# Kernel optimization log

Hardware: AMD Instinct MI355X
Metric: run time of the kernel (lower is better)

Reference implementation:

```python
import jax, jax.numpy as jnp
import numpy as np

D_MODEL = 1024
N_EXPERTS = 8
TOP_K = 2


def setup_inputs() -> dict:
    key = jax.random.key(0)
    ks = jax.random.split(key, 8)
    d, e = D_MODEL, N_EXPERTS
    s = 1.0 / np.sqrt(d)
    return {
        "x": jax.random.normal(ks[0], (4, 2048, d), dtype=jnp.float32),
        "W_gate": jax.random.uniform(ks[1], (d, e), jnp.float32, -s, s),
        "b_gate": jax.random.uniform(ks[2], (e,), jnp.float32, -s, s),
        "W1": jax.random.uniform(ks[3], (e, d, d), jnp.float32, -s, s),
        "b1": jax.random.uniform(ks[4], (e, d), jnp.float32, -s, s),
        "W2": jax.random.uniform(ks[5], (e, d, d), jnp.float32, -s, s),
        "b2": jax.random.uniform(ks[6], (e, d), jnp.float32, -s, s),
    }


def reference(x, W_gate, b_gate, W1, b1, W2, b2):
    B, T, d = x.shape
    xf = x.reshape(-1, d)  # [N, d], N = B*T
    # gating: raw linear scores, top-k selection; top-k raw scores are the
    # combine weights (original applies no softmax to gate scores)
    scores = xf @ W_gate + b_gate  # [N, E]
    topk_val, topk_idx = jax.lax.top_k(scores, TOP_K)  # [N, K]
    # scatter top-k weights into dense [N, E] combine matrix (indices distinct)
    onehot = jax.nn.one_hot(topk_idx, N_EXPERTS, dtype=xf.dtype)  # [N, K, E]
    w = jnp.einsum("nk,nke->ne", topk_val, onehot)  # [N, E]
    # run every expert MLP densely, then mask-combine (static shapes under jit)
    h = jax.nn.relu(jnp.einsum("nd,edh->neh", xf, W1) + b1)  # [N, E, d]
    y = jnp.einsum("neh,ehd->ned", h, W2) + b2  # [N, E, d]
    out = jnp.einsum("ned,ne->nd", y, w)  # weighted combine over experts
    return out.reshape(B, T, d)
```

## Files before the change

kernel.cpp:

```cpp
#include <hip/hip_runtime.h>
#include <hip/hip_bf16.h>


#define NTOK   8192
#define DM     1024
#define NE     8
#define BM     128
#define NSLOT  (NTOK * 2)
#define PADCAP (NSLOT + NE * BM)
#define MAXTILES (PADCAP / BM)

typedef __attribute__((ext_vector_type(8))) short  bf16x8;
typedef __attribute__((ext_vector_type(4))) float  f32x4;
typedef __attribute__((ext_vector_type(8))) unsigned short u16x8;

__device__ __forceinline__ unsigned short f2bf(float f) {
    union { float f; unsigned u; } v; v.f = f;
    unsigned r = v.u + 0x7fffu + ((v.u >> 16) & 1u);
    return (unsigned short)(r >> 16);
}

__device__ __forceinline__ void load_lds16(const ushort* g, ushort* l) {
    __builtin_amdgcn_global_load_lds(
        (const __attribute__((address_space(1))) unsigned int*)g,
        (__attribute__((address_space(3))) unsigned int*)l,
        16, 0, 0);
}

__global__ __launch_bounds__(256) void k_transpose2(const float* __restrict__ W1,
                                                    const float* __restrict__ W2,
                                                    ushort* __restrict__ w1t,
                                                    ushort* __restrict__ w2t,
                                                    int* __restrict__ counts) {
    int tid = threadIdx.x;
    if (blockIdx.x == 0 && blockIdx.y == 0 && blockIdx.z == 0 && tid < 16)
        counts[tid] = 0;
    int ez = blockIdx.z;
    const float* W = (ez < 8 ? W1 : W2) + (size_t)(ez & 7) * DM * DM;
    ushort* Wt = (ez < 8 ? w1t : w2t) + (size_t)(ez & 7) * DM * DM;
    __shared__ float t[64][65];
    int kt = blockIdx.y * 64, nt = blockIdx.x * 64;
    int r16 = tid >> 4, c4 = (tid & 15) * 4;
#pragma unroll
    for (int p = 0; p < 4; p++) {
        int k = p * 16 + r16;
        float4 v = *(const float4*)&W[(size_t)(kt + k) * DM + nt + c4];
        t[k][c4] = v.x; t[k][c4 + 1] = v.y; t[k][c4 + 2] = v.z; t[k][c4 + 3] = v.w;
    }
    __syncthreads();
    int n = tid >> 2, kb = (tid & 3) * 16;
#pragma unroll
    for (int h = 0; h < 2; h++) {
        int k0 = kb + h * 8;
        u16x8 o;
#pragma unroll
        for (int i = 0; i < 8; i++) o[i] = f2bf(t[k0 + i][n]);
        *(u16x8*)&Wt[(size_t)(nt + n) * DM + kt + k0] = o;
    }
}

__global__ __launch_bounds__(256) void k_gate(const float* __restrict__ x,
                                              const float* __restrict__ Wg,
                                              const float* __restrict__ bg,
                                              ushort* __restrict__ xb,
                                              int* __restrict__ tok_e,
                                              float* __restrict__ tok_w,
                                              int* __restrict__ counts,
                                              float* __restrict__ out,
                                              int* __restrict__ slot_token) {
    __shared__ float wgT[NE][DM];
    __shared__ int cnt[NE];
    int tid = threadIdx.x;
    if (tid < NE) cnt[tid] = 0;
    {
        float4 z4 = {0.f, 0.f, 0.f, 0.f};
        float4* orow = (float4*)(out + (size_t)blockIdx.x * 16 * DM);
#pragma unroll
        for (int i = 0; i < 16; i++) orow[i * 256 + tid] = z4;
        int s0 = blockIdx.x * (PADCAP / 512);
        for (int i = tid; i < PADCAP / 512; i += 256) slot_token[s0 + i] = -1;
    }
    for (int i = tid; i < DM * NE; i += 256) {
        int d = i >> 3, e = i & 7;
        wgT[e][d] = Wg[i];
    }
    __syncthreads();
    int wave = tid >> 6, lane = tid & 63;
    int n0 = (blockIdx.x * 4 + wave) * 4;
    const float4* xr[4];
#pragma unroll
    for (int t = 0; t < 4; t++) xr[t] = (const float4*)(x + (size_t)(n0 + t) * DM);

    float acc[4][NE];
#pragma unroll
    for (int t = 0; t < 4; t++)
#pragma unroll
        for (int e = 0; e < NE; e++) acc[t][e] = 0.f;

#pragma unroll
    for (int j = 0; j < 4; j++) {
        float4 xv[4];
#pragma unroll
        for (int t = 0; t < 4; t++) xv[t] = xr[t][j * 64 + lane];
#pragma unroll
        for (int t = 0; t < 4; t++) {
            ushort4 o;
            o.x = f2bf(xv[t].x); o.y = f2bf(xv[t].y);
            o.z = f2bf(xv[t].z); o.w = f2bf(xv[t].w);
            ((ushort4*)xb)[(size_t)(n0 + t) * (DM / 4) + j * 64 + lane] = o;
        }
#pragma unroll
        for (int e = 0; e < NE; e++) {
            float4 wv = ((const float4*)&wgT[e][0])[j * 64 + lane];
#pragma unroll
            for (int t = 0; t < 4; t++) {
                acc[t][e] += xv[t].x * wv.x + xv[t].y * wv.y
                           + xv[t].z * wv.z + xv[t].w * wv.w;
            }
        }
    }
#pragma unroll
    for (int t = 0; t < 4; t++)
#pragma unroll
        for (int e = 0; e < NE; e++) {
#pragma unroll
            for (int off = 32; off >= 1; off >>= 1)
                acc[t][e] += __shfl_xor(acc[t][e], off);
        }
    if (lane < 4) {
        int t = lane, n = n0 + t;
        float sc[NE];
#pragma unroll
        for (int e = 0; e < NE; e++) sc[e] = acc[t][e] + bg[e];
        int e0 = 0; float v0 = sc[0];
#pragma unroll
        for (int e = 1; e < NE; e++) if (sc[e] > v0) { v0 = sc[e]; e0 = e; }
        int e1 = -1; float v1 = -3.0e38f;
#pragma unroll
        for (int e = 0; e < NE; e++) if (e != e0 && sc[e] > v1) { v1 = sc[e]; e1 = e; }
        tok_e[2 * n] = e0;     tok_w[2 * n] = v0;
        tok_e[2 * n + 1] = e1; tok_w[2 * n + 1] = v1;
        atomicAdd(&cnt[e0], 1);
        atomicAdd(&cnt[e1], 1);
    }
    __syncthreads();
    if (tid < NE) atomicAdd(&counts[tid], cnt[tid]);
}

__global__ __launch_bounds__(256) void k_fillplan(const int* __restrict__ tok_e,
                                                  const float* __restrict__ tok_w,
                                                  const int* __restrict__ counts,
                                                  int* __restrict__ cursor,
                                                  int* __restrict__ slot_token,
                                                  float* __restrict__ slot_w,
                                                  int* __restrict__ tile_e,
                                                  int* __restrict__ tile_b,
                                                  int* __restrict__ ntiles) {
    __shared__ int lcnt[NE], lbase[NE];
    int tid = threadIdx.x;
    if (tid < NE) lcnt[tid] = 0;
    __syncthreads();
    int n = blockIdx.x * 256 + tid;
    int e0 = tok_e[2 * n],     e1 = tok_e[2 * n + 1];
    float w0 = tok_w[2 * n],   w1 = tok_w[2 * n + 1];
    int p0 = atomicAdd(&lcnt[e0], 1);
    int p1 = atomicAdd(&lcnt[e1], 1);
    __syncthreads();
    if (tid < NE) lbase[tid] = atomicAdd(&cursor[tid], lcnt[tid]);
    if (blockIdx.x == 0 && tid == 32) {
        int t = 0, o2 = 0;
        for (int e = 0; e < NE; e++) {
            int nt = (counts[e] + BM - 1) / BM;
            for (int i = 0; i < nt; i++) { tile_e[t] = e; tile_b[t] = o2 + i * BM; t++; }
            o2 += nt * BM;
        }
        *ntiles = t;
    }
    __syncthreads();
    int base[NE]; int off = 0;
#pragma unroll
    for (int e = 0; e < NE; e++) {
        base[e] = off;
        off += ((counts[e] + BM - 1) / BM) * BM;
    }
    int s0 = base[e0] + lbase[e0] + p0;
    slot_token[s0] = n; slot_w[s0] = w0;
    int s1 = base[e1] + lbase[e1] + p1;
    slot_token[s1] = n; slot_w[s1] = w1;
}

template <int PHASE>
__global__ __launch_bounds__(256) void k_gemm(const ushort* __restrict__ A,
                                              const ushort* __restrict__ Wt,
                                              const float* __restrict__ bias,
                                              const int* __restrict__ slot_token,
                                              const float* __restrict__ slot_w,
                                              const int* __restrict__ tile_e,
                                              const int* __restrict__ tile_b,
                                              const int* __restrict__ ntiles,
                                              ushort* __restrict__ Hout,
                                              float* __restrict__ out) {
    int flat = blockIdx.x;
    int wid = (flat & 7) * (MAXTILES * 2) + (flat >> 3);
    int t = wid >> 4;
    if (t >= *ntiles) return;
    int ncol0 = (wid & 15) << 6;
    int e = tile_e[t];
    int sbase = tile_b[t];

    __shared__ ushort As[2][4096];
    __shared__ ushort Bs[2][2048];

    int tid = threadIdx.x;
    int wave = tid >> 6, lane = tid & 63, quad = lane >> 4, lm = lane & 15;
    int wm = wave >> 1, wn = wave & 1;

    const ushort* Wte = Wt + (size_t)e * DM * DM;

    int sr = lane >> 2;
    int gseg = (lane & 3) ^ ((lane >> 4) & 3);
    const ushort* aptr[2];
    const ushort* bptr;
#pragma unroll
    for (int ci = 0; ci < 2; ci++) {
        int row = (wave * 2 + ci) * 16 + sr;
        int ar;
        if (PHASE == 1) {
            ar = slot_token[sbase + row];
            if (ar < 0) ar = 0;
        } else {
            ar = sbase + row;
        }
        aptr[ci] = A + (size_t)ar * DM + gseg * 8;
    }
    {
        int brow = wave * 16 + sr;
        bptr = Wte + (size_t)(ncol0 + brow) * DM + gseg * 8;
    }

    f32x4 acc[4][2];
#pragma unroll
    for (int i = 0; i < 4; i++)
#pragma unroll
        for (int j = 0; j < 2; j++) acc[i][j] = (f32x4){0.f, 0.f, 0.f, 0.f};

    int asel = ((quad ^ (lm >> 2)) & 3) * 8;
    int abase = (wm * 64 + lm) * 32 + asel;
    int bbase = (wn * 32 + lm) * 32 + asel;

#define ISSUE(buf, koff)                                              \
    do {                                                              \
        load_lds16(aptr[0] + (koff), &As[(buf)][(wave * 2 + 0) * 512]); \
        load_lds16(aptr[1] + (koff), &As[(buf)][(wave * 2 + 1) * 512]); \
        load_lds16(bptr + (koff), &Bs[(buf)][wave * 512]);            \
    } while (0)

#define COMPUTE(buf)                                                          \
    do {                                                                      \
        const ushort* Ab = As[(buf)];                                         \
        const ushort* Bb = Bs[(buf)];                                         \
        bf16x8 av[4], bv[2];                                                  \
        _Pragma("unroll")                                                     \
        for (int f = 0; f < 4; f++) av[f] = *(const bf16x8*)&Ab[abase + f * 512]; \
        _Pragma("unroll")                                                     \
        for (int f = 0; f < 2; f++) bv[f] = *(const bf16x8*)&Bb[bbase + f * 512]; \
        __builtin_amdgcn_s_setprio(1);                                        \
        _Pragma("unroll")                                                     \
        for (int fm = 0; fm < 4; fm++)                                        \
            _Pragma("unroll")                                                 \
            for (int fn = 0; fn < 2; fn++)                                    \
                acc[fm][fn] = __builtin_amdgcn_mfma_f32_16x16x32_bf16(        \
                    av[fm], bv[fn], acc[fm][fn], 0, 0, 0);                    \
        __builtin_amdgcn_s_setprio(0);                                        \
    } while (0)

    ISSUE(0, 0);
#pragma unroll 2
    for (int it = 0; it < 32; ++it) {
        if (it < 31) {
            ISSUE((it + 1) & 1, (it + 1) * 32);
            __builtin_amdgcn_s_waitcnt(0x0F73);
        } else {
            __builtin_amdgcn_s_waitcnt(0x0F70);
        }
        __builtin_amdgcn_s_barrier();
        __builtin_amdgcn_sched_barrier(0);
        COMPUTE(it & 1);
        __builtin_amdgcn_sched_barrier(0);
        __builtin_amdgcn_s_waitcnt(0xC07F);
        __builtin_amdgcn_s_barrier();
    }
#undef ISSUE
#undef COMPUTE

#pragma unroll
    for (int fm = 0; fm < 4; fm++) {
        int rowg = wm * 64 + fm * 16 + quad * 4;
        if (PHASE == 1) {
#pragma unroll
            for (int fn = 0; fn < 2; fn++) {
                int col = ncol0 + wn * 32 + fn * 16 + lm;
                float bv2 = bias[e * DM + col];
#pragma unroll
                for (int r = 0; r < 4; r++) {
                    float v = acc[fm][fn][r] + bv2;
                    v = fmaxf(v, 0.f);
                    Hout[(size_t)(sbase + rowg + r) * DM + col] = f2bf(v);
                }
            }
        } else {
            int tk[4]; float wv[4];
#pragma unroll
            for (int r = 0; r < 4; r++) {
                tk[r] = slot_token[sbase + rowg + r];
                wv[r] = slot_w[sbase + rowg + r];
            }
#pragma unroll
            for (int fn = 0; fn < 2; fn++) {
                int col = ncol0 + wn * 32 + fn * 16 + lm;
                float bv2 = bias[e * DM + col];
#pragma unroll
                for (int r = 0; r < 4; r++) {
                    if (tk[r] >= 0) {
                        float v = wv[r] * (acc[fm][fn][r] + bv2);
                        atomicAdd(&out[(size_t)tk[r] * DM + col], v);
                    }
                }
            }
        }
    }
}

extern "C" void kernel_launch(void* const* d_in, const int* in_sizes, int n_in,
                              void* d_out, int out_size, void* d_ws, size_t ws_size,
                              hipStream_t stream) {
    const float* x  = (const float*)d_in[0];
    const float* Wg = (const float*)d_in[1];
    const float* bg = (const float*)d_in[2];
    const float* W1 = (const float*)d_in[3];
    const float* b1 = (const float*)d_in[4];
    const float* W2 = (const float*)d_in[5];
    const float* b2 = (const float*)d_in[6];
    float* out = (float*)d_out;

    char* ws = (char*)d_ws;
    ushort* xb         = (ushort*)(ws + 0);
    ushort* w1t        = (ushort*)(ws + 16777216);
    ushort* w2t        = (ushort*)(ws + 33554432);
    ushort* H          = (ushort*)(ws + 50331648);
    int*    tok_e      = (int*)  (ws + 85983232);
    float*  tok_w      = (float*)(ws + 86048768);
    int*    slot_token = (int*)  (ws + 86114304);
    float*  slot_w     = (float*)(ws + 86183936);
    int*    counts     = (int*)  (ws + 86253568);
    int*    cursor     = counts + 8;
    int*    tile_e     = counts + 24;
    int*    tile_b     = tile_e + MAXTILES;
    int*    ntiles     = tile_b + MAXTILES;

    dim3 tg(16, 16, 16);
    k_transpose2<<<tg, 256, 0, stream>>>(W1, W2, w1t, w2t, counts);
    k_gate<<<NTOK / 16, 256, 0, stream>>>(x, Wg, bg, xb, tok_e, tok_w, counts,
                                          out, slot_token);
    k_fillplan<<<NTOK / 256, 256, 0, stream>>>(tok_e, tok_w, counts, cursor,
                                               slot_token, slot_w,
                                               tile_e, tile_b, ntiles);

    dim3 gg(16 * MAXTILES);
    k_gemm<1><<<gg, 256, 0, stream>>>(xb, w1t, b1, slot_token, slot_w,
                                      tile_e, tile_b, ntiles, H, nullptr);
    k_gemm<2><<<gg, 256, 0, stream>>>(H, w2t, b2, slot_token, slot_w,
                                      tile_e, tile_b, ntiles, nullptr, out);
}
```

Before: 331.4 us.

## Merge transpose and gate kernels, use per-block counts, halve GEMM grid

Fuses the weight transpose/convert kernel and the gating kernel into one launch, with blocks split by index, which removes a kernel launch and its serialization. Global atomic expert counts are replaced by per-block count arrays that the fill-plan kernel reduces itself. The GEMM grid is halved and each block now loops over two tiles, which cuts the number of early-exiting blocks but lowers the parallelism available per wave of work. The shared-memory footprint of the merged kernel is set by the larger gate path, which may reduce occupancy for the transpose blocks.

Result: slower. 342.4 us (+3.3%).

```diff
diff --git a/kernel.cpp b/kernel.cpp
--- a/kernel.cpp
+++ b/kernel.cpp
@@ -9,6 +9,7 @@
 #define NSLOT  (NTOK * 2)
 #define PADCAP (NSLOT + NE * BM)
 #define MAXTILES (PADCAP / BM)
+#define NGATE  512
 
 typedef __attribute__((ext_vector_type(8))) short  bf16x8;
 typedef __attribute__((ext_vector_type(4))) float  f32x4;
@@ -27,58 +28,61 @@
         16, 0, 0);
 }
 
-__global__ __launch_bounds__(256) void k_transpose2(const float* __restrict__ W1,
-                                                    const float* __restrict__ W2,
-                                                    ushort* __restrict__ w1t,
-                                                    ushort* __restrict__ w2t,
-                                                    int* __restrict__ counts) {
-    int tid = threadIdx.x;
-    if (blockIdx.x == 0 && blockIdx.y == 0 && blockIdx.z == 0 && tid < 16)
-        counts[tid] = 0;
-    int ez = blockIdx.z;
-    const float* W = (ez < 8 ? W1 : W2) + (size_t)(ez & 7) * DM * DM;
-    ushort* Wt = (ez < 8 ? w1t : w2t) + (size_t)(ez & 7) * DM * DM;
-    __shared__ float t[64][65];
-    int kt = blockIdx.y * 64, nt = blockIdx.x * 64;
-    int r16 = tid >> 4, c4 = (tid & 15) * 4;
-#pragma unroll
-    for (int p = 0; p < 4; p++) {
-        int k = p * 16 + r16;
-        float4 v = *(const float4*)&W[(size_t)(kt + k) * DM + nt + c4];
-        t[k][c4] = v.x; t[k][c4 + 1] = v.y; t[k][c4 + 2] = v.z; t[k][c4 + 3] = v.w;
-    }
-    __syncthreads();
-    int n = tid >> 2, kb = (tid & 3) * 16;
-#pragma unroll
-    for (int h = 0; h < 2; h++) {
-        int k0 = kb + h * 8;
-        u16x8 o;
-#pragma unroll
-        for (int i = 0; i < 8; i++) o[i] = f2bf(t[k0 + i][n]);
-        *(u16x8*)&Wt[(size_t)(nt + n) * DM + kt + k0] = o;
-    }
-}
-
-__global__ __launch_bounds__(256) void k_gate(const float* __restrict__ x,
+__global__ __launch_bounds__(256) void k_prep(const float* __restrict__ W1,
+                                              const float* __restrict__ W2,
+                                              ushort* __restrict__ w1t,
+                                              ushort* __restrict__ w2t,
+                                              const float* __restrict__ x,
                                               const float* __restrict__ Wg,
                                               const float* __restrict__ bg,
                                               ushort* __restrict__ xb,
                                               int* __restrict__ tok_e,
                                               float* __restrict__ tok_w,
-                                              int* __restrict__ counts,
+                                              int* __restrict__ gcnt,
                                               float* __restrict__ out,
-                                              int* __restrict__ slot_token) {
-    __shared__ float wgT[NE][DM];
+                                              int* __restrict__ slot_token,
+                                              int* __restrict__ cursor) {
+    __shared__ float smem[NE * DM];
     __shared__ int cnt[NE];
-    int tid = threadIdx.x;
+    int gb = blockIdx.x, tid = threadIdx.x;
+
+    if (gb >= NGATE) {
+        int tb = gb - NGATE;
+        int ez = tb >> 8;
+        const float* W = (ez < 8 ? W1 : W2) + (size_t)(ez & 7) * DM * DM;
+        ushort* Wt = (ez < 8 ? w1t : w2t) + (size_t)(ez & 7) * DM * DM;
+        float (*t)[65] = reinterpret_cast<float(*)[65]>(smem);
+        int kt = ((tb >> 4) & 15) * 64, nt = (tb & 15) * 64;
+        int r16 = tid >> 4, c4 = (tid & 15) * 4;
+#pragma unroll
+        for (int p = 0; p < 4; p++) {
+            int k = p * 16 + r16;
+            float4 v = *(const float4*)&W[(size_t)(kt + k) * DM + nt + c4];
+            t[k][c4] = v.x; t[k][c4 + 1] = v.y; t[k][c4 + 2] = v.z; t[k][c4 + 3] = v.w;
+        }
+        __syncthreads();
+        int n = tid >> 2, kb = (tid & 3) * 16;
+#pragma unroll
+        for (int h = 0; h < 2; h++) {
+            int k0 = kb + h * 8;
+            u16x8 o;
+#pragma unroll
+            for (int i = 0; i < 8; i++) o[i] = f2bf(t[k0 + i][n]);
+            *(u16x8*)&Wt[(size_t)(nt + n) * DM + kt + k0] = o;
+        }
+        return;
+    }
+
+    float (*wgT)[DM] = reinterpret_cast<float(*)[DM]>(smem);
+    if (gb == 0 && tid < NE) cursor[tid] = 0;
     if (tid < NE) cnt[tid] = 0;
     {
         float4 z4 = {0.f, 0.f, 0.f, 0.f};
-        float4* orow = (float4*)(out + (size_t)blockIdx.x * 16 * DM);
+        float4* orow = (float4*)(out + (size_t)gb * 16 * DM);
 #pragma unroll
         for (int i = 0; i < 16; i++) orow[i * 256 + tid] = z4;
-        int s0 = blockIdx.x * (PADCAP / 512);
-        for (int i = tid; i < PADCAP / 512; i += 256) slot_token[s0 + i] = -1;
+        int s0 = gb * (PADCAP / NGATE);
+        for (int i = tid; i < PADCAP / NGATE; i += 256) slot_token[s0 + i] = -1;
     }
     for (int i = tid; i < DM * NE; i += 256) {
         int d = i >> 3, e = i & 7;
@@ -86,7 +90,7 @@
     }
     __syncthreads();
     int wave = tid >> 6, lane = tid & 63;
-    int n0 = (blockIdx.x * 4 + wave) * 4;
+    int n0 = (gb * 4 + wave) * 4;
     const float4* xr[4];
 #pragma unroll
     for (int t = 0; t < 4; t++) xr[t] = (const float4*)(x + (size_t)(n0 + t) * DM);
@@ -144,22 +148,40 @@
         atomicAdd(&cnt[e1], 1);
     }
     __syncthreads();
-    if (tid < NE) atomicAdd(&counts[tid], cnt[tid]);
+    if (tid < NE) gcnt[gb * NE + tid] = cnt[tid];
 }
 
 __global__ __launch_bounds__(256) void k_fillplan(const int* __restrict__ tok_e,
                                                   const float* __restrict__ tok_w,
-                                                  const int* __restrict__ counts,
+                                                  const int* __restrict__ gcnt,
                                                   int* __restrict__ cursor,
                                                   int* __restrict__ slot_token,
                                                   float* __restrict__ slot_w,
                                                   int* __restrict__ tile_e,
                                                   int* __restrict__ tile_b,
                                                   int* __restrict__ ntiles) {
-    __shared__ int lcnt[NE], lbase[NE];
+    __shared__ int lcnt[NE], lbase[NE], wsum[4][NE];
     int tid = threadIdx.x;
     if (tid < NE) lcnt[tid] = 0;
-    __syncthreads();
+    int tot[NE];
+#pragma unroll
+    for (int e = 0; e < NE; e++) tot[e] = 0;
+    for (int r = tid; r < NGATE; r += 256)
+#pragma unroll
+        for (int e = 0; e < NE; e++) tot[e] += gcnt[r * NE + e];
+#pragma unroll
+    for (int e = 0; e < NE; e++)
+#pragma unroll
+        for (int off = 32; off >= 1; off >>= 1) tot[e] += __shfl_xor(tot[e], off);
+    int wave = tid >> 6, lane = tid & 63;
+    if (lane == 0)
+#pragma unroll
+        for (int e = 0; e < NE; e++) wsum[wave][e] = tot[e];
+    __syncthreads();
+#pragma unroll
+    for (int e = 0; e < NE; e++)
+        tot[e] = wsum[0][e] + wsum[1][e] + wsum[2][e] + wsum[3][e];
+
     int n = blockIdx.x * 256 + tid;
     int e0 = tok_e[2 * n],     e1 = tok_e[2 * n + 1];
     float w0 = tok_w[2 * n],   w1 = tok_w[2 * n + 1];
@@ -170,7 +192,7 @@
     if (blockIdx.x == 0 && tid == 32) {
         int t = 0, o2 = 0;
         for (int e = 0; e < NE; e++) {
-            int nt = (counts[e] + BM - 1) / BM;
+            int nt = (tot[e] + BM - 1) / BM;
             for (int i = 0; i < nt; i++) { tile_e[t] = e; tile_b[t] = o2 + i * BM; t++; }
             o2 += nt * BM;
         }
@@ -181,7 +203,7 @@
 #pragma unroll
     for (int e = 0; e < NE; e++) {
         base[e] = off;
-        off += ((counts[e] + BM - 1) / BM) * BM;
+        off += ((tot[e] + BM - 1) / BM) * BM;
     }
     int s0 = base[e0] + lbase[e0] + p0;
     slot_token[s0] = n; slot_w[s0] = w0;
@@ -200,53 +222,20 @@
                                               const int* __restrict__ ntiles,
                                               ushort* __restrict__ Hout,
                                               float* __restrict__ out) {
-    int flat = blockIdx.x;
-    int wid = (flat & 7) * (MAXTILES * 2) + (flat >> 3);
-    int t = wid >> 4;
-    if (t >= *ntiles) return;
-    int ncol0 = (wid & 15) << 6;
-    int e = tile_e[t];
-    int sbase = tile_b[t];
-
     __shared__ ushort As[2][4096];
     __shared__ ushort Bs[2][2048];
 
     int tid = threadIdx.x;
     int wave = tid >> 6, lane = tid & 63, quad = lane >> 4, lm = lane & 15;
     int wm = wave >> 1, wn = wave & 1;
-
-    const ushort* Wte = Wt + (size_t)e * DM * DM;
-
     int sr = lane >> 2;
     int gseg = (lane & 3) ^ ((lane >> 4) & 3);
-    const ushort* aptr[2];
-    const ushort* bptr;
-#pragma unroll
-    for (int ci = 0; ci < 2; ci++) {
-        int row = (wave * 2 + ci) * 16 + sr;
-        int ar;
-        if (PHASE == 1) {
-            ar = slot_token[sbase + row];
-            if (ar < 0) ar = 0;
-        } else {
-            ar = sbase + row;
-        }
-        aptr[ci] = A + (size_t)ar * DM + gseg * 8;
-    }
-    {
-        int brow = wave * 16 + sr;
-        bptr = Wte + (size_t)(ncol0 + brow) * DM + gseg * 8;
-    }
-
-    f32x4 acc[4][2];
-#pragma unroll
-    for (int i = 0; i < 4; i++)
-#pragma unroll
-        for (int j = 0; j < 2; j++) acc[i][j] = (f32x4){0.f, 0.f, 0.f, 0.f};
-
     int asel = ((quad ^ (lm >> 2)) & 3) * 8;
     int abase = (wm * 64 + lm) * 32 + asel;
     int bbase = (wn * 32 + lm) * 32 + asel;
+
+    int xcd = blockIdx.x & 7, slot = blockIdx.x >> 3;
+    int ntv = *ntiles;
 
 #define ISSUE(buf, koff)                                              \
     do {                                                              \
@@ -274,61 +263,97 @@
         __builtin_amdgcn_s_setprio(0);                                        \
     } while (0)
 
-    ISSUE(0, 0);
+#pragma unroll 1
+    for (int j = 0; j < 2; ++j) {
+        int wid = xcd * 272 + slot + 136 * j;
+        int t = wid >> 4;
+        if (t >= ntv) continue;
+        int ncol0 = (wid & 15) << 6;
+        int e = tile_e[t];
+        int sbase = tile_b[t];
+        const ushort* Wte = Wt + (size_t)e * DM * DM;
+
+        const ushort* aptr[2];
+        const ushort* bptr;
+#pragma unroll
+        for (int ci = 0; ci < 2; ci++) {
+            int row = (wave * 2 + ci) * 16 + sr;
+            int ar;
+            if (PHASE == 1) {
+                ar = slot_token[sbase + row];
+                if (ar < 0) ar = 0;
+            } else {
+                ar = sbase + row;
+            }
+            aptr[ci] = A + (size_t)ar * DM + gseg * 8;
+        }
+        {
+            int brow = wave * 16 + sr;
+            bptr = Wte + (size_t)(ncol0 + brow) * DM + gseg * 8;
+        }
+
+        f32x4 acc[4][2];
+#pragma unroll
+        for (int i = 0; i < 4; i++)
+#pragma unroll
+            for (int jj = 0; jj < 2; jj++) acc[i][jj] = (f32x4){0.f, 0.f, 0.f, 0.f};
+
+        ISSUE(0, 0);
 #pragma unroll 2
-    for (int it = 0; it < 32; ++it) {
-        if (it < 31) {
-            ISSUE((it + 1) & 1, (it + 1) * 32);
-            __builtin_amdgcn_s_waitcnt(0x0F73);
-        } else {
-            __builtin_amdgcn_s_waitcnt(0x0F70);
-        }
-        __builtin_amdgcn_s_barrier();
-        __builtin_amdgcn_sched_barrier(0);
-        COMPUTE(it & 1);
-        __builtin_amdgcn_sched_barrier(0);
-        __builtin_amdgcn_s_waitcnt(0xC07F);
-        __builtin_amdgcn_s_barrier();
-    }
-#undef ISSUE
-#undef COMPUTE
-
-#pragma unroll
-    for (int fm = 0; fm < 4; fm++) {
-        int rowg = wm * 64 + fm * 16 + quad * 4;
-        if (PHASE == 1) {
-#pragma unroll
-            for (int fn = 0; fn < 2; fn++) {
-                int col = ncol0 + wn * 32 + fn * 16 + lm;
-                float bv2 = bias[e * DM + col];
+        for (int it = 0; it < 32; ++it) {
+            if (it < 31) {
+                ISSUE((it + 1) & 1, (it + 1) * 32);
+                __builtin_amdgcn_s_waitcnt(0x0F73);
+            } else {
+                __builtin_amdgcn_s_waitcnt(0x0F70);
+            }
+            __builtin_amdgcn_s_barrier();
+            __builtin_amdgcn_sched_barrier(0);
+            COMPUTE(it & 1);
+            __builtin_amdgcn_sched_barrier(0);
+            __builtin_amdgcn_s_waitcnt(0xC07F);
+            __builtin_amdgcn_s_barrier();
+        }
+
+#pragma unroll
+        for (int fm = 0; fm < 4; fm++) {
+            int rowg = wm * 64 + fm * 16 + quad * 4;
+            if (PHASE == 1) {
+#pragma unroll
+                for (int fn = 0; fn < 2; fn++) {
+                    int col = ncol0 + wn * 32 + fn * 16 + lm;
+                    float bv2 = bias[e * DM + col];
+#pragma unroll
+                    for (int r = 0; r < 4; r++) {
+                        float v = acc[fm][fn][r] + bv2;
+                        v = fmaxf(v, 0.f);
+                        Hout[(size_t)(sbase + rowg + r) * DM + col] = f2bf(v);
+                    }
+                }
+            } else {
+                int tk[4]; float wv[4];
 #pragma unroll
                 for (int r = 0; r < 4; r++) {
-                    float v = acc[fm][fn][r] + bv2;
-                    v = fmaxf(v, 0.f);
-                    Hout[(size_t)(sbase + rowg + r) * DM + col] = f2bf(v);
+                    tk[r] = slot_token[sbase + rowg + r];
+                    wv[r] = slot_w[sbase + rowg + r];
                 }
-            }
-        } else {
-            int tk[4]; float wv[4];
-#pragma unroll
-            for (int r = 0; r < 4; r++) {
-                tk[r] = slot_token[sbase + rowg + r];
-                wv[r] = slot_w[sbase + rowg + r];
-            }
-#pragma unroll
-            for (int fn = 0; fn < 2; fn++) {
-                int col = ncol0 + wn * 32 + fn * 16 + lm;
-                float bv2 = bias[e * DM + col];
-#pragma unroll
-                for (int r = 0; r < 4; r++) {
-                    if (tk[r] >= 0) {
-                        float v = wv[r] * (acc[fm][fn][r] + bv2);
-                        atomicAdd(&out[(size_t)tk[r] * DM + col], v);
+#pragma unroll
+                for (int fn = 0; fn < 2; fn++) {
+                    int col = ncol0 + wn * 32 + fn * 16 + lm;
+                    float bv2 = bias[e * DM + col];
+#pragma unroll
+                    for (int r = 0; r < 4; r++) {
+                        if (tk[r] >= 0) {
+                            float v = wv[r] * (acc[fm][fn][r] + bv2);
+                            atomicAdd(&out[(size_t)tk[r] * DM + col], v);
+                        }
                     }
                 }
             }
         }
     }
+#undef ISSUE
+#undef COMPUTE
 }
 
 extern "C" void kernel_launch(void* const* d_in, const int* in_sizes, int n_in,
@@ -352,21 +377,20 @@
     float*  tok_w      = (float*)(ws + 86048768);
     int*    slot_token = (int*)  (ws + 86114304);
     float*  slot_w     = (float*)(ws + 86183936);
-    int*    counts     = (int*)  (ws + 86253568);
-    int*    cursor     = counts + 8;
-    int*    tile_e     = counts + 24;
+    int*    cursor     = (int*)  (ws + 86253568);
+    int*    tile_e     = cursor + 16;
     int*    tile_b     = tile_e + MAXTILES;
     int*    ntiles     = tile_b + MAXTILES;
-
-    dim3 tg(16, 16, 16);
-    k_transpose2<<<tg, 256, 0, stream>>>(W1, W2, w1t, w2t, counts);
-    k_gate<<<NTOK / 16, 256, 0, stream>>>(x, Wg, bg, xb, tok_e, tok_w, counts,
-                                          out, slot_token);
-    k_fillplan<<<NTOK / 256, 256, 0, stream>>>(tok_e, tok_w, counts, cursor,
+    int*    gcnt       = (int*)  (ws + 86257664);
+
+    k_prep<<<NGATE + 4096, 256, 0, stream>>>(W1, W2, w1t, w2t,
+                                             x, Wg, bg, xb, tok_e, tok_w,
+                                             gcnt, out, slot_token, cursor);
+    k_fillplan<<<NTOK / 256, 256, 0, stream>>>(tok_e, tok_w, gcnt, cursor,
                                                slot_token, slot_w,
                                                tile_e, tile_b, ntiles);
 
-    dim3 gg(16 * MAXTILES);
+    dim3 gg(8 * MAXTILES);
     k_gemm<1><<<gg, 256, 0, stream>>>(xb, w1t, b1, slot_token, slot_w,
                                       tile_e, tile_b, ntiles, H, nullptr);
     k_gemm<2><<<gg, 256, 0, stream>>>(H, w2t, b2, slot_token, slot_w,
```
